# Optimization experiments

Hardware: AMD Instinct MI355X
Metric: run time of the kernel (lower is better)

Reference implementation:

```python
import jax, jax.numpy as jnp
import numpy as np

NUM_IN = 1024
NUM_OUT = 2048
N_EXPERTS = 16
N_TOKENS = 65536  # N_expanded, equally split across experts (4096 per expert)


def setup_inputs() -> dict:
    key = jax.random.key(0)
    k1, k2, k3 = jax.random.split(key, 3)
    sorted_features = jax.random.normal(k1, (N_TOKENS, NUM_IN), dtype=jnp.float32)
    # expert ids in sorted order: equal split of N_TOKENS across N_EXPERTS
    expert_ids_sorted = jnp.repeat(jnp.arange(N_EXPERTS, dtype=jnp.int32), N_TOKENS // N_EXPERTS)
    # routing weights: std = 1/sqrt(num_out*experts + num_in), bias std = 1
    w_std = 1.0 / (NUM_OUT * N_EXPERTS + NUM_IN) ** 0.5
    routing_matrix = jax.random.normal(k2, (NUM_IN, NUM_OUT, N_EXPERTS), dtype=jnp.float32) * w_std
    routing_bias = jax.random.normal(k3, (NUM_OUT, N_EXPERTS), dtype=jnp.float32)
    return {
        "sorted_features": sorted_features,
        "expert_ids_sorted": expert_ids_sorted,
        "routing_matrix": routing_matrix,
        "routing_bias": routing_bias,
    }


def reference(sorted_features, expert_ids_sorted, routing_matrix, routing_bias):
    """forward_expert_batched with equal split_sizes: grouped GEMM + bias, silu at end."""
    E = routing_matrix.shape[2]
    N, d_in = sorted_features.shape
    # tokens are sorted by expert id with equal counts -> static reshape
    x = sorted_features.reshape(E, N // E, d_in)          # [E, n, in]
    W = jnp.transpose(routing_matrix, (2, 0, 1))          # [E, in, out]
    b = routing_bias.T[:, None, :]                        # [E, 1, out]
    y = jnp.einsum("eni,eio->eno", x, W) + b              # grouped GEMM + per-expert bias
    return jax.nn.silu(y).reshape(N, -1)                  # activation applied once at end
```

## Files before the change

### kernel.cpp

```cpp
#include <hip/hip_runtime.h>
#include <hip/hip_bf16.h>


#define E_ 16
#define DIN 1024
#define DOUT 2048
#define NTOK 65536
#define NPE (NTOK / E_)
#define NKT (DIN / 64)
#define NI (NKT / 2)

typedef __attribute__((ext_vector_type(8))) short short8;
typedef __attribute__((ext_vector_type(4))) float f32x4;

__device__ __forceinline__ unsigned short f2bf(float f) {
  union { float f; unsigned int u; } v; v.f = f;
  unsigned int u = v.u;
  return (unsigned short)((u + 0x7fffu + ((u >> 16) & 1u)) >> 16);
}

__device__ __forceinline__ void gload_lds16(const void* g, void* l) {
  __builtin_amdgcn_global_load_lds(
      (const __attribute__((address_space(1))) void*)g,
      (__attribute__((address_space(3))) void*)l, 16, 0, 0);
}

__global__ __launch_bounds__(256)
void prep_x(const float* __restrict__ x, unsigned short* __restrict__ xs) {
  const int nunits = NTOK * (DIN / 8);
  for (int u = blockIdx.x * 256 + threadIdx.x; u < nunits; u += gridDim.x * 256) {
    const int m = u >> 7;
    const int j = u & 127;
    const float4* src = (const float4*)(x + (size_t)m * DIN + j * 8);
    const float4 a = src[0], b = src[1];
    uint4 v;
    v.x = f2bf(a.x) | ((unsigned)f2bf(a.y) << 16);
    v.y = f2bf(a.z) | ((unsigned)f2bf(a.w) << 16);
    v.z = f2bf(b.x) | ((unsigned)f2bf(b.y) << 16);
    v.w = f2bf(b.z) | ((unsigned)f2bf(b.w) << 16);
    const int js = (j & ~7) | ((j & 7) ^ (m & 7));
    *(uint4*)(xs + (size_t)m * DIN + js * 8) = v;
  }
}

template <bool SWZ>
__global__ __launch_bounds__(256)
void prep_w(const float* __restrict__ W, unsigned short* __restrict__ Wt) {
  __shared__ unsigned short tile[16][32][33];
  const int k0 = (blockIdx.x >> 6) * 32;
  const int o0 = (blockIdx.x & 63) * 32;
  const int tid = threadIdx.x;

  for (int p = tid; p < 1024; p += 256) {
    const int k = p >> 5, o = p & 31;
    const float4* src = (const float4*)(W + ((size_t)(k0 + k) * DOUT + (o0 + o)) * 16);
    float4 v0 = src[0], v1 = src[1], v2 = src[2], v3 = src[3];
    const float vv[16] = {v0.x, v0.y, v0.z, v0.w, v1.x, v1.y, v1.z, v1.w,
                          v2.x, v2.y, v2.z, v2.w, v3.x, v3.y, v3.z, v3.w};
    #pragma unroll
    for (int e = 0; e < 16; ++e) tile[e][k][o] = f2bf(vv[e]);
  }
  __syncthreads();
  for (int c = tid; c < 2048; c += 256) {
    const int kc = c & 3, o = (c >> 2) & 31, e = c >> 7;
    unsigned short vals[8];
    #pragma unroll
    for (int j = 0; j < 8; ++j) vals[j] = tile[e][kc * 8 + j][o];
    uint4 wv;
    wv.x = vals[0] | ((unsigned)vals[1] << 16);
    wv.y = vals[2] | ((unsigned)vals[3] << 16);
    wv.z = vals[4] | ((unsigned)vals[5] << 16);
    wv.w = vals[6] | ((unsigned)vals[7] << 16);
    const int jb = (k0 >> 3) + kc;
    const int jbs = SWZ ? ((jb & ~7) | ((jb & 7) ^ (o & 7))) : jb;
    *(uint4*)(Wt + (size_t)e * (DOUT * DIN) + (size_t)(o0 + o) * DIN + jbs * 8) = wv;
  }
}

__global__ __launch_bounds__(512, 2)
void moe_gemm8(const unsigned short* __restrict__ xs, const unsigned short* __restrict__ Wt,
               const float* __restrict__ bias, float* __restrict__ out) {
  extern __shared__ char smem[];

  const int bid = blockIdx.x;
  const int swz = (bid & 7) * 256 + (bid >> 3);
  const int e  = swz >> 7;
  const int mb = (swz >> 3) & 15;
  const int nb = swz & 7;
  const int row0 = e * NPE + mb * 256;
  const int col0 = nb * 256;

  const int tid = threadIdx.x;
  const int lane = tid & 63;
  const int w = tid >> 6;
  const int wm = w >> 2, wn = w & 3;
  const int l15 = lane & 15;

  const char* xa  = (const char*)xs + (size_t)row0 * (DIN * 2);
  const char* wbg = (const char*)(Wt + (size_t)e * (DOUT * DIN) + (size_t)col0 * DIN);

  const int crow0 = w * 16 + (lane >> 3);
  const int kb16  = (lane & 7) * 16;
  const int dch0  = w * 2048;

  const int hi16  = (lane >> 4) << 4;
  const int sw7   = (lane & 7) << 4;
  const int koff0 = (0   | hi16) ^ sw7;
  const int koff1 = (64  | hi16) ^ sw7;

  f32x4 acc[8][4];
  #pragma unroll
  for (int i = 0; i < 8; ++i)
    #pragma unroll
    for (int j = 0; j < 4; ++j) acc[i][j] = (f32x4){0.f, 0.f, 0.f, 0.f};

  short8 a[8], b[8];

#define STAGE_A(slot, half, kt) do { \
    gload_lds16(xa + (size_t)((half) * 128 + crow0) * (DIN * 2) + (kt) * 128 + kb16, \
                smem + (slot) * 32768 + (half) * 16384 + dch0); \
    gload_lds16(xa + (size_t)((half) * 128 + crow0 + 8) * (DIN * 2) + (kt) * 128 + kb16, \
                smem + (slot) * 32768 + (half) * 16384 + dch0 + 1024); \
  } while (0)

#define STAGE_B(slot, half, kt) do { \
    gload_lds16(wbg + (size_t)((half) * 128 + crow0) * (DIN * 2) + (kt) * 128 + kb16, \
                smem + 65536 + (slot) * 32768 + (half) * 16384 + dch0); \
    gload_lds16(wbg + (size_t)((half) * 128 + crow0 + 8) * (DIN * 2) + (kt) * 128 + kb16, \
                smem + 65536 + (slot) * 32768 + (half) * 16384 + dch0 + 1024); \
  } while (0)

#define READ_A(slot, qm_) do { \
    _Pragma("unroll") \
    for (int mf = 0; mf < 4; ++mf) { \
      const int r_ = wm * 128 + (qm_) * 64 + mf * 16 + l15; \
      const char* p_ = smem + (slot) * 32768 + r_ * 128; \
      a[mf * 2 + 0] = *(const short8*)(p_ + koff0); \
      a[mf * 2 + 1] = *(const short8*)(p_ + koff1); \
    } \
  } while (0)

#define READ_B(slot, qn_) do { \
    _Pragma("unroll") \
    for (int nf = 0; nf < 2; ++nf) { \
      const int c_ = wn * 64 + (qn_) * 32 + nf * 16 + l15; \
      const char* p_ = smem + 65536 + (slot) * 32768 + c_ * 128; \
      b[(qn_) * 4 + nf * 2 + 0] = *(const short8*)(p_ + koff0); \
      b[(qn_) * 4 + nf * 2 + 1] = *(const short8*)(p_ + koff1); \
    } \
  } while (0)

#define MFMA_Q(qm_, qn_) do { \
    __builtin_amdgcn_s_setprio(1); \
    _Pragma("unroll") \
    for (int mf = 0; mf < 4; ++mf) \
      _Pragma("unroll") \
      for (int nf = 0; nf < 2; ++nf) { \
        acc[(qm_) * 4 + mf][(qn_) * 2 + nf] = __builtin_amdgcn_mfma_f32_16x16x32_bf16( \
            a[mf * 2 + 0], b[((qn_) * 2 + nf) * 2 + 0], acc[(qm_) * 4 + mf][(qn_) * 2 + nf], 0, 0, 0); \
        acc[(qm_) * 4 + mf][(qn_) * 2 + nf] = __builtin_amdgcn_mfma_f32_16x16x32_bf16( \
            a[mf * 2 + 1], b[((qn_) * 2 + nf) * 2 + 1], acc[(qm_) * 4 + mf][(qn_) * 2 + nf], 0, 0, 0); \
      } \
    __builtin_amdgcn_s_setprio(0); \
  } while (0)

#define BAR() do { asm volatile("s_barrier" ::: "memory"); __builtin_amdgcn_sched_barrier(0); } while (0)
#define VMCNT4() asm volatile("s_waitcnt vmcnt(4)" ::: "memory")
#define VMCNT0() asm volatile("s_waitcnt vmcnt(0)" ::: "memory")

  STAGE_A(0, 0, 0); STAGE_A(0, 1, 0); STAGE_B(0, 0, 0); STAGE_B(0, 1, 0);
  STAGE_B(1, 0, 1); STAGE_B(1, 1, 1);
  VMCNT4();
  BAR();

  for (int i = 0; i < NI; ++i) {
    const int t2 = 2 * i + 2, t3 = 2 * i + 3;
    const bool pf = (i < NI - 1);
    READ_A(0, 0); READ_B(0, 0);
    STAGE_A(1, 0, 2 * i + 1);
    BAR(); MFMA_Q(0, 0); BAR();
    READ_B(0, 1);
    STAGE_A(1, 1, 2 * i + 1);
    BAR(); MFMA_Q(0, 1); BAR();
    READ_A(0, 1);
    if (pf) STAGE_B(0, 0, t2);
    BAR(); MFMA_Q(1, 1); BAR();
    if (pf) STAGE_B(0, 1, t2);
    BAR(); MFMA_Q(1, 0);
    if (pf) { VMCNT4(); } else { VMCNT0(); }
    BAR();
    READ_A(1, 0); READ_B(1, 0);
    if (pf) STAGE_A(0, 0, t2);
    BAR(); MFMA_Q(0, 0); BAR();
    READ_B(1, 1);
    if (pf) STAGE_A(0, 1, t2);
    BAR(); MFMA_Q(0, 1); BAR();
    READ_A(1, 1);
    if (pf) STAGE_B(1, 0, t3);
    BAR(); MFMA_Q(1, 1); BAR();
    if (pf) STAGE_B(1, 1, t3);
    BAR(); MFMA_Q(1, 0);
    if (pf) { VMCNT4(); }
    BAR();
  }

#undef STAGE_A
#undef STAGE_B
#undef READ_A
#undef READ_B
#undef MFMA_Q
#undef BAR
#undef VMCNT4
#undef VMCNT0

  #pragma unroll
  for (int nr = 0; nr < 4; ++nr) {
    const int col = col0 + wn * 64 + nr * 16 + l15;
    const float bv = bias[col * 16 + e];
    #pragma unroll
    for (int mr = 0; mr < 8; ++mr) {
      const int row = row0 + wm * 128 + mr * 16 + ((lane >> 4) << 2);
      const f32x4 v = acc[mr][nr];
      #pragma unroll
      for (int rr = 0; rr < 4; ++rr) {
        const float y = v[rr] + bv;
        out[(size_t)(row + rr) * DOUT + col] = y * (1.0f / (1.0f + __expf(-y)));
      }
    }
  }
}

__global__ __launch_bounds__(256, 4)
void moe_gemm_s(const unsigned short* __restrict__ xs, const unsigned short* __restrict__ Wt,
                const float* __restrict__ bias, float* __restrict__ out) {
  __shared__ unsigned short sA[128 * 64];
  __shared__ unsigned short sB[128 * 64];

  const int bid = blockIdx.x;
  const int swz = (bid & 7) * 1024 + (bid >> 3);
  const int e  = swz >> 9;
  const int mb = (swz >> 4) & 31;
  const int nb = swz & 15;
  const int row0 = e * NPE + mb * 128;
  const int col0 = nb * 128;

  const int tid = threadIdx.x;
  const int lane = tid & 63;
  const int w = tid >> 6;
  const int wm = w >> 1, wn = w & 1;

  const char* xa = (const char*)xs + (size_t)row0 * (DIN * 2);
  const char* wb = (const char*)(Wt + (size_t)e * (DOUT * DIN) + (size_t)col0 * DIN);
  const int lrow8 = lane >> 3;
  const int lk = (lane & 7) * 16;

  f32x4 acc[4][4];
  #pragma unroll
  for (int i = 0; i < 4; ++i)
    #pragma unroll
    for (int j = 0; j < 4; ++j) acc[i][j] = (f32x4){0.f, 0.f, 0.f, 0.f};

  for (int kt = 0; kt < NKT; ++kt) {
    __syncthreads();
    #pragma unroll
    for (int i = 0; i < 4; ++i) {
      const int c = w * 4 + i;
      const int r = c * 8 + lrow8;
      gload_lds16(xa + (size_t)r * (DIN * 2) + kt * 128 + lk, (char*)sA + c * 1024);
      gload_lds16(wb + (size_t)r * (DIN * 2) + kt * 128 + lk, (char*)sB + c * 1024);
    }
    __syncthreads();
    #pragma unroll
    for (int ks = 0; ks < 2; ++ks) {
      short8 av[4], bv[4];
      const int hib = ks * 64 + ((lane >> 4) << 4);
      #pragma unroll
      for (int mf = 0; mf < 4; ++mf) {
        const int r = wm * 64 + mf * 16 + (lane & 15);
        av[mf] = *(const short8*)((const char*)sA + r * 128 + (hib ^ ((r & 7) << 4)));
      }
      #pragma unroll
      for (int nf = 0; nf < 4; ++nf) {
        const int o = wn * 64 + nf * 16 + (lane & 15);
        bv[nf] = *(const short8*)((const char*)sB + o * 128 + (hib ^ ((o & 7) << 4)));
      }
      #pragma unroll
      for (int mf = 0; mf < 4; ++mf)
        #pragma unroll
        for (int nf = 0; nf < 4; ++nf)
          acc[mf][nf] = __builtin_amdgcn_mfma_f32_16x16x32_bf16(av[mf], bv[nf], acc[mf][nf], 0, 0, 0);
    }
  }

  #pragma unroll
  for (int nf = 0; nf < 4; ++nf) {
    const int col = col0 + wn * 64 + nf * 16 + (lane & 15);
    const float bv = bias[col * 16 + e];
    #pragma unroll
    for (int mf = 0; mf < 4; ++mf) {
      const int row = row0 + wm * 64 + mf * 16 + ((lane >> 4) << 2);
      const f32x4 v = acc[mf][nf];
      #pragma unroll
      for (int r = 0; r < 4; ++r) {
        const float y = v[r] + bv;
        out[(size_t)(row + r) * DOUT + col] = y * (1.0f / (1.0f + __expf(-y)));
      }
    }
  }
}

#define BM 128
#define BN 128
#define BK 64
#define LDA 72

__global__ __launch_bounds__(256, 2)
void moe_gemm_f32a(const float* __restrict__ x, const unsigned short* __restrict__ Wt,
                   const float* __restrict__ bias, float* __restrict__ out) {
  __shared__ unsigned short sA[2][BM * LDA];
  __shared__ unsigned short sB[2][BN * BK];

  const int bid = blockIdx.x;
  const int swz = (bid & 7) * 1024 + (bid >> 3);
  const int e  = swz >> 9;
  const int mb = (swz >> 4) & 31;
  const int nb = swz & 15;
  const int row0 = e * NPE + mb * BM;
  const int col0 = nb * BN;

  const int tid = threadIdx.x;
  const int lane = tid & 63;
  const int w = tid >> 6;
  const int wm = w >> 1, wn = w & 1;

  const float* xb = x + (size_t)row0 * DIN;
  const char* wbase = (const char*)(Wt + (size_t)e * (DOUT * DIN) + (size_t)col0 * DIN);

  f32x4 acc[4][4];
  #pragma unroll
  for (int i = 0; i < 4; ++i)
    #pragma unroll
    for (int j = 0; j < 4; ++j) acc[i][j] = (f32x4){0.f, 0.f, 0.f, 0.f};

  float4 ar[8];

  #pragma unroll
  for (int i = 0; i < 8; ++i) {
    const int c = tid + i * 256;
    ar[i] = *(const float4*)(xb + (size_t)(c >> 4) * DIN + (c & 15) * 4);
  }
  #pragma unroll
  for (int j = 0; j < 4; ++j) {
    const int ch = w * 4 + j;
    const int L = ch * 1024 + lane * 16;
    const int o_l = L >> 7;
    const int kb = (L & 127) ^ ((o_l & 7) << 4);
    gload_lds16(wbase + (size_t)o_l * (DIN * 2) + kb, (char*)(&sB[0][0]) + ch * 1024);
  }
  #pragma unroll
  for (int i = 0; i < 8; ++i) {
    const int c = tid + i * 256;
    uint2 hv;
    hv.x = f2bf(ar[i].x) | ((unsigned)f2bf(ar[i].y) << 16);
    hv.y = f2bf(ar[i].z) | ((unsigned)f2bf(ar[i].w) << 16);
    *(uint2*)((char*)(&sA[0][0]) + (c >> 4) * (LDA * 2) + (c & 15) * 8) = hv;
  }
  __syncthreads();

  int cur = 0;
  for (int kt = 0; kt < NKT; ++kt) {
    const int nxt = cur ^ 1;
    if (kt + 1 < NKT) {
      #pragma unroll
      for (int i = 0; i < 8; ++i) {
        const int c = tid + i * 256;
        ar[i] = *(const float4*)(xb + (size_t)(c >> 4) * DIN + (kt + 1) * BK + (c & 15) * 4);
      }
      #pragma unroll
      for (int j = 0; j < 4; ++j) {
        const int ch = w * 4 + j;
        const int L = ch * 1024 + lane * 16;
        const int o_l = L >> 7;
        const int kb = (L & 127) ^ ((o_l & 7) << 4);
        gload_lds16(wbase + (size_t)o_l * (DIN * 2) + (size_t)(kt + 1) * (BK * 2) + kb,
                    (char*)(&sB[nxt][0]) + ch * 1024);
      }
    }
    const char* Ab = (const char*)(&sA[cur][0]);
    const char* Bb = (const char*)(&sB[cur][0]);
    #pragma unroll
    for (int ks = 0; ks < 2; ++ks) {
      short8 av[4], bv[4];
      #pragma unroll
      for (int mf = 0; mf < 4; ++mf) {
        const int r = wm * 64 + mf * 16 + (lane & 15);
        av[mf] = *(const short8*)(Ab + r * (LDA * 2) + ks * 64 + ((lane >> 4) << 4));
      }
      #pragma unroll
      for (int nf = 0; nf < 4; ++nf) {
        const int o = wn * 64 + nf * 16 + (lane & 15);
        const int kb = (ks * 64 + ((lane >> 4) << 4)) ^ ((o & 7) << 4);
        bv[nf] = *(const short8*)(Bb + o * 128 + kb);
      }
      #pragma unroll
      for (int mf = 0; mf < 4; ++mf)
        #pragma unroll
        for (int nf = 0; nf < 4; ++nf)
          acc[mf][nf] = __builtin_amdgcn_mfma_f32_16x16x32_bf16(av[mf], bv[nf], acc[mf][nf], 0, 0, 0);
    }
    if (kt + 1 < NKT) {
      #pragma unroll
      for (int i = 0; i < 8; ++i) {
        const int c = tid + i * 256;
        uint2 hv;
        hv.x = f2bf(ar[i].x) | ((unsigned)f2bf(ar[i].y) << 16);
        hv.y = f2bf(ar[i].z) | ((unsigned)f2bf(ar[i].w) << 16);
        *(uint2*)((char*)(&sA[nxt][0]) + (c >> 4) * (LDA * 2) + (c & 15) * 8) = hv;
      }
    }
    __syncthreads();
    cur = nxt;
  }

  #pragma unroll
  for (int nf = 0; nf < 4; ++nf) {
    const int col = col0 + wn * 64 + nf * 16 + (lane & 15);
    const float bv = bias[col * 16 + e];
    #pragma unroll
    for (int mf = 0; mf < 4; ++mf) {
      const int row = row0 + wm * 64 + mf * 16 + ((lane >> 4) << 2);
      const f32x4 v = acc[mf][nf];
      #pragma unroll
      for (int r = 0; r < 4; ++r) {
        const float y = v[r] + bv;
        out[(size_t)(row + r) * DOUT + col] = y * (1.0f / (1.0f + __expf(-y)));
      }
    }
  }
}

extern "C" void kernel_launch(void* const* d_in, const int* in_sizes, int n_in,
                              void* d_out, int out_size, void* d_ws, size_t ws_size,
                              hipStream_t stream) {
  const float* x    = (const float*)d_in[0];
  const float* W    = (const float*)d_in[2];
  const float* bias = (const float*)d_in[3];
  float* out = (float*)d_out;

  const size_t wt_bytes = (size_t)E_ * DOUT * DIN * 2;
  const size_t xs_bytes = (size_t)NTOK * DIN * 2;

  unsigned short* Wt = (unsigned short*)d_ws;

  if (ws_size >= wt_bytes + xs_bytes) {
    unsigned short* xsw = (unsigned short*)((char*)d_ws + wt_bytes);
    prep_x<<<2048, 256, 0, stream>>>(x, xsw);
    prep_w<true><<<2048, 256, 0, stream>>>(W, Wt);
    static const bool lds_ok =
        (hipFuncSetAttribute(reinterpret_cast<const void*>(moe_gemm8),
                             hipFuncAttributeMaxDynamicSharedMemorySize, 131072) == hipSuccess);
    if (lds_ok) {
      moe_gemm8<<<2048, 512, 131072, stream>>>(xsw, Wt, bias, out);
    } else {
      moe_gemm_s<<<8192, 256, 0, stream>>>(xsw, Wt, bias, out);
    }
  } else {
    prep_w<false><<<2048, 256, 0, stream>>>(W, Wt);
    moe_gemm_f32a<<<8192, 256, 0, stream>>>(x, Wt, bias, out);
  }
}
```

Baseline: 506.6 us.

## Fuse prep kernels into one launch and restructure GEMM into half-phase schedule

Merges the activation and weight bf16 conversion kernels into a single launch, with the block index selecting the role, so the two prep passes can overlap and one launch is saved. The main GEMM loop moves from four quarter-tile MFMA phases per k-tile to two half-tile phases: all B fragments are read at once and staging loads are issued in pairs. This halves the number of barriers per k-tile at the cost of more live B registers and coarser interleaving of loads with MFMAs. The fallback path gets a plain, unswizzled weight-prep kernel.

```diff
diff --git a/kernel.cpp b/kernel.cpp
--- a/kernel.cpp
+++ b/kernel.cpp
@@ -26,60 +26,59 @@
 }
 
 __global__ __launch_bounds__(256)
-void prep_x(const float* __restrict__ x, unsigned short* __restrict__ xs) {
-  const int nunits = NTOK * (DIN / 8);
-  for (int u = blockIdx.x * 256 + threadIdx.x; u < nunits; u += gridDim.x * 256) {
-    const int m = u >> 7;
-    const int j = u & 127;
-    const float4* src = (const float4*)(x + (size_t)m * DIN + j * 8);
-    const float4 a = src[0], b = src[1];
-    uint4 v;
-    v.x = f2bf(a.x) | ((unsigned)f2bf(a.y) << 16);
-    v.y = f2bf(a.z) | ((unsigned)f2bf(a.w) << 16);
-    v.z = f2bf(b.x) | ((unsigned)f2bf(b.y) << 16);
-    v.w = f2bf(b.z) | ((unsigned)f2bf(b.w) << 16);
-    const int js = (j & ~7) | ((j & 7) ^ (m & 7));
-    *(uint4*)(xs + (size_t)m * DIN + js * 8) = v;
-  }
-}
-
-template <bool SWZ>
-__global__ __launch_bounds__(256)
-void prep_w(const float* __restrict__ W, unsigned short* __restrict__ Wt) {
+void prep_fused(const float* __restrict__ x, unsigned short* __restrict__ xs,
+                const float* __restrict__ W, unsigned short* __restrict__ Wt) {
   __shared__ unsigned short tile[16][32][33];
-  const int k0 = (blockIdx.x >> 6) * 32;
-  const int o0 = (blockIdx.x & 63) * 32;
   const int tid = threadIdx.x;
-
-  for (int p = tid; p < 1024; p += 256) {
-    const int k = p >> 5, o = p & 31;
-    const float4* src = (const float4*)(W + ((size_t)(k0 + k) * DOUT + (o0 + o)) * 16);
-    float4 v0 = src[0], v1 = src[1], v2 = src[2], v3 = src[3];
-    const float vv[16] = {v0.x, v0.y, v0.z, v0.w, v1.x, v1.y, v1.z, v1.w,
-                          v2.x, v2.y, v2.z, v2.w, v3.x, v3.y, v3.z, v3.w};
-    #pragma unroll
-    for (int e = 0; e < 16; ++e) tile[e][k][o] = f2bf(vv[e]);
-  }
-  __syncthreads();
-  for (int c = tid; c < 2048; c += 256) {
-    const int kc = c & 3, o = (c >> 2) & 31, e = c >> 7;
-    unsigned short vals[8];
-    #pragma unroll
-    for (int j = 0; j < 8; ++j) vals[j] = tile[e][kc * 8 + j][o];
-    uint4 wv;
-    wv.x = vals[0] | ((unsigned)vals[1] << 16);
-    wv.y = vals[2] | ((unsigned)vals[3] << 16);
-    wv.z = vals[4] | ((unsigned)vals[5] << 16);
-    wv.w = vals[6] | ((unsigned)vals[7] << 16);
-    const int jb = (k0 >> 3) + kc;
-    const int jbs = SWZ ? ((jb & ~7) | ((jb & 7) ^ (o & 7))) : jb;
-    *(uint4*)(Wt + (size_t)e * (DOUT * DIN) + (size_t)(o0 + o) * DIN + jbs * 8) = wv;
+  if (blockIdx.x < 2048) {
+    const int bid = blockIdx.x;
+    const int k0 = (bid >> 6) * 32;
+    const int o0 = (bid & 63) * 32;
+    for (int p = tid; p < 1024; p += 256) {
+      const int k = p >> 5, o = p & 31;
+      const float4* src = (const float4*)(W + ((size_t)(k0 + k) * DOUT + (o0 + o)) * 16);
+      float4 v0 = src[0], v1 = src[1], v2 = src[2], v3 = src[3];
+      const float vv[16] = {v0.x, v0.y, v0.z, v0.w, v1.x, v1.y, v1.z, v1.w,
+                            v2.x, v2.y, v2.z, v2.w, v3.x, v3.y, v3.z, v3.w};
+      #pragma unroll
+      for (int e = 0; e < 16; ++e) tile[e][k][o] = f2bf(vv[e]);
+    }
+    __syncthreads();
+    for (int c = tid; c < 2048; c += 256) {
+      const int kc = c & 3, o = (c >> 2) & 31, e = c >> 7;
+      unsigned short vals[8];
+      #pragma unroll
+      for (int j = 0; j < 8; ++j) vals[j] = tile[e][kc * 8 + j][o];
+      uint4 wv;
+      wv.x = vals[0] | ((unsigned)vals[1] << 16);
+      wv.y = vals[2] | ((unsigned)vals[3] << 16);
+      wv.z = vals[4] | ((unsigned)vals[5] << 16);
+      wv.w = vals[6] | ((unsigned)vals[7] << 16);
+      const int jb = (k0 >> 3) + kc;
+      const int jbs = (jb & ~7) | ((jb & 7) ^ (o & 7));
+      *(uint4*)(Wt + (size_t)e * (DOUT * DIN) + (size_t)(o0 + o) * DIN + jbs * 8) = wv;
+    }
+  } else {
+    const int nunits = NTOK * (DIN / 8);
+    for (int u = (blockIdx.x - 2048) * 256 + tid; u < nunits; u += 2048 * 256) {
+      const int m = u >> 7;
+      const int j = u & 127;
+      const float4* src = (const float4*)(x + (size_t)m * DIN + j * 8);
+      const float4 a = src[0], b = src[1];
+      uint4 v;
+      v.x = f2bf(a.x) | ((unsigned)f2bf(a.y) << 16);
+      v.y = f2bf(a.z) | ((unsigned)f2bf(a.w) << 16);
+      v.z = f2bf(b.x) | ((unsigned)f2bf(b.y) << 16);
+      v.w = f2bf(b.z) | ((unsigned)f2bf(b.w) << 16);
+      const int js = (j & ~7) | ((j & 7) ^ (m & 7));
+      *(uint4*)(xs + (size_t)m * DIN + js * 8) = v;
+    }
   }
 }
 
 __global__ __launch_bounds__(512, 2)
-void moe_gemm8(const unsigned short* __restrict__ xs, const unsigned short* __restrict__ Wt,
-               const float* __restrict__ bias, float* __restrict__ out) {
+void moe_gemm4p(const unsigned short* __restrict__ xs, const unsigned short* __restrict__ Wt,
+                const float* __restrict__ bias, float* __restrict__ out) {
   extern __shared__ char smem[];
 
   const int bid = blockIdx.x;
@@ -105,8 +104,8 @@
 
   const int hi16  = (lane >> 4) << 4;
   const int sw7   = (lane & 7) << 4;
-  const int koff0 = (0   | hi16) ^ sw7;
-  const int koff1 = (64  | hi16) ^ sw7;
+  const int koff0 = (0  | hi16) ^ sw7;
+  const int koff1 = (64 | hi16) ^ sw7;
 
   f32x4 acc[8][4];
   #pragma unroll
@@ -140,26 +139,26 @@
     } \
   } while (0)
 
-#define READ_B(slot, qn_) do { \
+#define READ_B_ALL(slot) do { \
     _Pragma("unroll") \
-    for (int nf = 0; nf < 2; ++nf) { \
-      const int c_ = wn * 64 + (qn_) * 32 + nf * 16 + l15; \
+    for (int nf = 0; nf < 4; ++nf) { \
+      const int c_ = wn * 64 + nf * 16 + l15; \
       const char* p_ = smem + 65536 + (slot) * 32768 + c_ * 128; \
-      b[(qn_) * 4 + nf * 2 + 0] = *(const short8*)(p_ + koff0); \
-      b[(qn_) * 4 + nf * 2 + 1] = *(const short8*)(p_ + koff1); \
+      b[nf * 2 + 0] = *(const short8*)(p_ + koff0); \
+      b[nf * 2 + 1] = *(const short8*)(p_ + koff1); \
     } \
   } while (0)
 
-#define MFMA_Q(qm_, qn_) do { \
+#define MFMA_QM(qm_) do { \
     __builtin_amdgcn_s_setprio(1); \
     _Pragma("unroll") \
     for (int mf = 0; mf < 4; ++mf) \
       _Pragma("unroll") \
-      for (int nf = 0; nf < 2; ++nf) { \
-        acc[(qm_) * 4 + mf][(qn_) * 2 + nf] = __builtin_amdgcn_mfma_f32_16x16x32_bf16( \
-            a[mf * 2 + 0], b[((qn_) * 2 + nf) * 2 + 0], acc[(qm_) * 4 + mf][(qn_) * 2 + nf], 0, 0, 0); \
-        acc[(qm_) * 4 + mf][(qn_) * 2 + nf] = __builtin_amdgcn_mfma_f32_16x16x32_bf16( \
-            a[mf * 2 + 1], b[((qn_) * 2 + nf) * 2 + 1], acc[(qm_) * 4 + mf][(qn_) * 2 + nf], 0, 0, 0); \
+      for (int nf = 0; nf < 4; ++nf) { \
+        acc[(qm_) * 4 + mf][nf] = __builtin_amdgcn_mfma_f32_16x16x32_bf16( \
+            a[mf * 2 + 0], b[nf * 2 + 0], acc[(qm_) * 4 + mf][nf], 0, 0, 0); \
+        acc[(qm_) * 4 + mf][nf] = __builtin_amdgcn_mfma_f32_16x16x32_bf16( \
+            a[mf * 2 + 1], b[nf * 2 + 1], acc[(qm_) * 4 + mf][nf], 0, 0, 0); \
       } \
     __builtin_amdgcn_s_setprio(0); \
   } while (0)
@@ -168,7 +167,8 @@
 #define VMCNT4() asm volatile("s_waitcnt vmcnt(4)" ::: "memory")
 #define VMCNT0() asm volatile("s_waitcnt vmcnt(0)" ::: "memory")
 
-  STAGE_A(0, 0, 0); STAGE_A(0, 1, 0); STAGE_B(0, 0, 0); STAGE_B(0, 1, 0);
+  STAGE_B(0, 0, 0); STAGE_B(0, 1, 0);
+  STAGE_A(0, 0, 0); STAGE_A(0, 1, 0);
   STAGE_B(1, 0, 1); STAGE_B(1, 1, 1);
   VMCNT4();
   BAR();
@@ -176,30 +176,20 @@
   for (int i = 0; i < NI; ++i) {
     const int t2 = 2 * i + 2, t3 = 2 * i + 3;
     const bool pf = (i < NI - 1);
-    READ_A(0, 0); READ_B(0, 0);
-    STAGE_A(1, 0, 2 * i + 1);
-    BAR(); MFMA_Q(0, 0); BAR();
-    READ_B(0, 1);
-    STAGE_A(1, 1, 2 * i + 1);
-    BAR(); MFMA_Q(0, 1); BAR();
+    READ_A(0, 0); READ_B_ALL(0);
+    STAGE_A(1, 0, 2 * i + 1); STAGE_A(1, 1, 2 * i + 1);
+    BAR(); MFMA_QM(0); BAR();
     READ_A(0, 1);
-    if (pf) STAGE_B(0, 0, t2);
-    BAR(); MFMA_Q(1, 1); BAR();
-    if (pf) STAGE_B(0, 1, t2);
-    BAR(); MFMA_Q(1, 0);
+    if (pf) { STAGE_B(0, 0, t2); STAGE_B(0, 1, t2); }
+    BAR(); MFMA_QM(1);
     if (pf) { VMCNT4(); } else { VMCNT0(); }
     BAR();
-    READ_A(1, 0); READ_B(1, 0);
-    if (pf) STAGE_A(0, 0, t2);
-    BAR(); MFMA_Q(0, 0); BAR();
-    READ_B(1, 1);
-    if (pf) STAGE_A(0, 1, t2);
-    BAR(); MFMA_Q(0, 1); BAR();
+    READ_A(1, 0); READ_B_ALL(1);
+    if (pf) { STAGE_A(0, 0, t2); STAGE_A(0, 1, t2); }
+    BAR(); MFMA_QM(0); BAR();
     READ_A(1, 1);
-    if (pf) STAGE_B(1, 0, t3);
-    BAR(); MFMA_Q(1, 1); BAR();
-    if (pf) STAGE_B(1, 1, t3);
-    BAR(); MFMA_Q(1, 0);
+    if (pf) { STAGE_B(1, 0, t3); STAGE_B(1, 1, t3); }
+    BAR(); MFMA_QM(1);
     if (pf) { VMCNT4(); }
     BAR();
   }
@@ -207,8 +197,8 @@
 #undef STAGE_A
 #undef STAGE_B
 #undef READ_A
-#undef READ_B
-#undef MFMA_Q
+#undef READ_B_ALL
+#undef MFMA_QM
 #undef BAR
 #undef VMCNT4
 #undef VMCNT0
@@ -314,6 +304,36 @@
 #define BK 64
 #define LDA 72
 
+__global__ void prep_w_plain(const float* __restrict__ W, unsigned short* __restrict__ Wt) {
+  __shared__ unsigned short tile[16][32][33];
+  const int k0 = (blockIdx.x >> 6) * 32;
+  const int o0 = (blockIdx.x & 63) * 32;
+  const int tid = threadIdx.x;
+
+  for (int p = tid; p < 1024; p += 256) {
+    const int k = p >> 5, o = p & 31;
+    const float4* src = (const float4*)(W + ((size_t)(k0 + k) * DOUT + (o0 + o)) * 16);
+    float4 v0 = src[0], v1 = src[1], v2 = src[2], v3 = src[3];
+    const float vv[16] = {v0.x, v0.y, v0.z, v0.w, v1.x, v1.y, v1.z, v1.w,
+                          v2.x, v2.y, v2.z, v2.w, v3.x, v3.y, v3.z, v3.w};
+    #pragma unroll
+    for (int e = 0; e < 16; ++e) tile[e][k][o] = f2bf(vv[e]);
+  }
+  __syncthreads();
+  for (int c = tid; c < 2048; c += 256) {
+    const int kc = c & 3, o = (c >> 2) & 31, e = c >> 7;
+    unsigned short vals[8];
+    #pragma unroll
+    for (int j = 0; j < 8; ++j) vals[j] = tile[e][kc * 8 + j][o];
+    uint4 wv;
+    wv.x = vals[0] | ((unsigned)vals[1] << 16);
+    wv.y = vals[2] | ((unsigned)vals[3] << 16);
+    wv.z = vals[4] | ((unsigned)vals[5] << 16);
+    wv.w = vals[6] | ((unsigned)vals[7] << 16);
+    *(uint4*)(Wt + (size_t)e * (DOUT * DIN) + (size_t)(o0 + o) * DIN + k0 + kc * 8) = wv;
+  }
+}
+
 __global__ __launch_bounds__(256, 2)
 void moe_gemm_f32a(const float* __restrict__ x, const unsigned short* __restrict__ Wt,
                    const float* __restrict__ bias, float* __restrict__ out) {
@@ -454,18 +474,17 @@
 
   if (ws_size >= wt_bytes + xs_bytes) {
     unsigned short* xsw = (unsigned short*)((char*)d_ws + wt_bytes);
-    prep_x<<<2048, 256, 0, stream>>>(x, xsw);
-    prep_w<true><<<2048, 256, 0, stream>>>(W, Wt);
+    prep_fused<<<4096, 256, 0, stream>>>(x, xsw, W, Wt);
     static const bool lds_ok =
-        (hipFuncSetAttribute(reinterpret_cast<const void*>(moe_gemm8),
+        (hipFuncSetAttribute(reinterpret_cast<const void*>(moe_gemm4p),
                              hipFuncAttributeMaxDynamicSharedMemorySize, 131072) == hipSuccess);
     if (lds_ok) {
-      moe_gemm8<<<2048, 512, 131072, stream>>>(xsw, Wt, bias, out);
+      moe_gemm4p<<<2048, 512, 131072, stream>>>(xsw, Wt, bias, out);
     } else {
       moe_gemm_s<<<8192, 256, 0, stream>>>(xsw, Wt, bias, out);
     }
   } else {
-    prep_w<false><<<2048, 256, 0, stream>>>(W, Wt);
+    prep_w_plain<<<2048, 256, 0, stream>>>(W, Wt);
     moe_gemm_f32a<<<8192, 256, 0, stream>>>(x, Wt, bias, out);
   }
 }
```

Measured after the change: 541.2 us. 1.07x slower.
